# Kernel optimization log

Measured on AMD Instinct MI355X. Metric: run time of the kernel, lower is better.

The kernel has to match this reference:

```python
import jax, jax.numpy as jnp
import numpy as np
import math

B, S = 2, 2048
V, D, H, L, DFF = 1024, 512, 8, 6, 2048
DK = D // H
EPS = 1e-5


def _pos_encoding(seq_len, d_model, dtype):
    pos = jnp.arange(seq_len, dtype=jnp.float32)[:, None]
    div = jnp.exp(jnp.arange(0, d_model, 2, dtype=jnp.float32) * (-math.log(10000.0) / d_model))
    pe = jnp.zeros((seq_len, d_model), dtype=jnp.float32)
    pe = pe.at[:, 0::2].set(jnp.sin(pos * div))
    pe = pe.at[:, 1::2].set(jnp.cos(pos * div))
    return pe.astype(dtype)


def _layernorm(x, w, b):
    mu = jnp.mean(x, axis=-1, keepdims=True)
    var = jnp.mean(jnp.square(x - mu), axis=-1, keepdims=True)
    return (x - mu) * jax.lax.rsqrt(var + EPS) * w + b


def setup_inputs() -> dict:
    key = jax.random.key(0)
    ks = jax.random.split(key, 20)
    s = 0.02
    inp = {
        "input_ids": jax.random.randint(ks[0], (B, S), 1, V),
        "emb": jax.random.normal(ks[1], (V, D)) * s,
        # linear weights stored (in, out) so y = x @ W + b
        "wq": jax.random.normal(ks[2], (L, D, D)) * s,
        "bq": jnp.zeros((L, D)),
        "wk": jax.random.normal(ks[3], (L, D, D)) * s,
        "bk": jnp.zeros((L, D)),
        "wv": jax.random.normal(ks[4], (L, D, D)) * s,
        "bv": jnp.zeros((L, D)),
        "wo": jax.random.normal(ks[5], (L, D, D)) * (s / math.sqrt(2 * L)),
        "bo": jnp.zeros((L, D)),
        "ln1_w": jnp.ones((L, D)), "ln1_b": jnp.zeros((L, D)),
        "ln2_w": jnp.ones((L, D)), "ln2_b": jnp.zeros((L, D)),
        "w1": jax.random.normal(ks[6], (L, D, DFF)) * s,
        "b1": jnp.zeros((L, DFF)),
        "w2": jax.random.normal(ks[7], (L, DFF, D)) * (s / math.sqrt(2 * L)),
        "b2": jnp.zeros((L, D)),
        "out_w": jax.random.normal(ks[8], (D, V)) * s,
        "out_b": jnp.zeros((V,)),
    }
    return inp


def reference(input_ids, emb, wq, bq, wk, bk, wv, bv, wo, bo,
              ln1_w, ln1_b, ln2_w, ln2_b, w1, b1, w2, b2, out_w, out_b):
    pad_mask = (input_ids != 0)                              # [B,S] attend where True
    x = emb[input_ids]                                       # [B,S,D]
    x = x + _pos_encoding(S, D, x.dtype)[None, :, :]
    causal = jnp.tril(jnp.ones((S, S), dtype=bool))          # [S,S]
    mask = causal[None, None, :, :] & pad_mask[:, None, None, :]  # [B,1,S,S]
    scale = 1.0 / math.sqrt(DK)
    for l in range(L):
        h = _layernorm(x, ln1_w[l], ln1_b[l])
        q = (h @ wq[l] + bq[l]).reshape(B, S, H, DK)
        k = (h @ wk[l] + bk[l]).reshape(B, S, H, DK)
        v = (h @ wv[l] + bv[l]).reshape(B, S, H, DK)
        scores = jnp.einsum('bqhd,bkhd->bhqk', q, k) * scale
        scores = jnp.where(mask, scores, -jnp.inf)
        attn = jax.nn.softmax(scores, axis=-1)
        o = jnp.einsum('bhqk,bkhd->bqhd', attn, v).reshape(B, S, D)
        x = o @ wo[l] + bo[l]                                # NOTE: no residual on attention (faithful)
        h2 = _layernorm(x, ln2_w[l], ln2_b[l])
        ff = jax.nn.relu(h2 @ w1[l] + b1[l]) @ w2[l] + b2[l]
        x = x + ff
    logits = x @ out_w + out_b                               # [B,S,V]
    return logits
```

## Files before the change

### kernel.cpp

```cpp
#include <hip/hip_runtime.h>
#include <hip/hip_bf16.h>

#define B_ 2
#define S_ 2048
#define V_ 1024
#define D_ 512
#define H_ 8
#define L_ 6
#define DFF_ 2048
#define DK_ 64
#define MROWS (B_*S_)
#define NEGINF (-__builtin_inff())

typedef __hip_bfloat16 bf16;
typedef __bf16 bf16x8 __attribute__((ext_vector_type(8)));
typedef float f32x4 __attribute__((ext_vector_type(4)));
typedef unsigned short us8 __attribute__((ext_vector_type(8)));
typedef unsigned short us2 __attribute__((ext_vector_type(2)));

__device__ __forceinline__ float bf2f(unsigned short u) {
    return __uint_as_float(((unsigned int)u) << 16);
}
__device__ __forceinline__ unsigned short f2b(float x) {
    unsigned int u = __float_as_uint(x);
    return (unsigned short)((u + 0x7FFFu + ((u >> 16) & 1u)) >> 16);
}
__device__ __forceinline__ float ldin(const void* p, size_t i, int bf) {
    return bf ? bf2f(((const unsigned short*)p)[i]) : ((const float*)p)[i];
}

__global__ void detect_kernel(const unsigned int* __restrict__ w, int* __restrict__ flag) {
    if (threadIdx.x == 0) flag[0] = (w[0] == 0x3F800000u) ? 0 : 1;
}

__global__ __launch_bounds__(256) void embed_kernel(const int* __restrict__ ids,
        const void* __restrict__ emb, float* __restrict__ x, const int* __restrict__ dtf)
{
    const int bf = dtf[0];
    int tid = blockIdx.x * 256 + threadIdx.x;
    int d = tid % D_;
    int bs = tid / D_;
    int s = bs % S_;
    int id = ids[bs];
    float e = ldin(emb, (size_t)id * D_ + d, bf);
    int i2 = d & ~1;
    float div = expf((float)i2 * (-9.210340371976184f / (float)D_));
    float ang = (float)s * div;
    float pe = (d & 1) ? cosf(ang) : sinf(ang);
    x[tid] = e + pe;
}

__global__ __launch_bounds__(256) void ln_kernel(const float* __restrict__ x,
        const void* __restrict__ w, const void* __restrict__ b, size_t off,
        unsigned short* __restrict__ out, const int* __restrict__ dtf)
{
    const int bf = dtf[0];
    __shared__ float red[256];
    const int row = blockIdx.x;
    const int tid = threadIdx.x;
    const float* xr = x + (size_t)row * D_;
    float v0 = xr[tid], v1 = xr[tid + 256];
    red[tid] = v0 + v1; __syncthreads();
    for (int s = 128; s > 0; s >>= 1) { if (tid < s) red[tid] += red[tid + s]; __syncthreads(); }
    float mu = red[0] * (1.f / D_); __syncthreads();
    float d0 = v0 - mu, d1 = v1 - mu;
    red[tid] = d0 * d0 + d1 * d1; __syncthreads();
    for (int s = 128; s > 0; s >>= 1) { if (tid < s) red[tid] += red[tid + s]; __syncthreads(); }
    float var = red[0] * (1.f / D_);
    float rstd = rsqrtf(var + 1e-5f);
    unsigned short* orow = out + (size_t)row * D_;
    orow[tid]       = f2b(d0 * rstd * ldin(w, off + tid, bf)       + ldin(b, off + tid, bf));
    orow[tid + 256] = f2b(d1 * rstd * ldin(w, off + tid + 256, bf) + ldin(b, off + tid + 256, bf));
}

__device__ __forceinline__ void tr_tile(const void* src, size_t off, int K, int N,
        unsigned short* dst, int k0, int n0, int bf, unsigned short (*T)[72])
{
    const int t = threadIdx.x;
    const int r = t >> 2, c = (t & 3) * 16;
    size_t e = off + (size_t)(k0 + r) * N + n0 + c;
    us8 u0, u1;
    if (bf) {
        u0 = *(const us8*)((const unsigned short*)src + e);
        u1 = *(const us8*)((const unsigned short*)src + e + 8);
    } else {
        const float* p = (const float*)src + e;
        float4 f0 = *(const float4*)p, f1 = *(const float4*)(p + 4);
        float4 f2 = *(const float4*)(p + 8), f3 = *(const float4*)(p + 12);
        u0[0]=f2b(f0.x); u0[1]=f2b(f0.y); u0[2]=f2b(f0.z); u0[3]=f2b(f0.w);
        u0[4]=f2b(f1.x); u0[5]=f2b(f1.y); u0[6]=f2b(f1.z); u0[7]=f2b(f1.w);
        u1[0]=f2b(f2.x); u1[1]=f2b(f2.y); u1[2]=f2b(f2.z); u1[3]=f2b(f2.w);
        u1[4]=f2b(f3.x); u1[5]=f2b(f3.y); u1[6]=f2b(f3.z); u1[7]=f2b(f3.w);
    }
    *(us8*)&T[r][c] = u0;
    *(us8*)&T[r][c + 8] = u1;
    __syncthreads();
    us8 o0, o1;
    #pragma unroll
    for (int i = 0; i < 8; ++i) { o0[i] = T[c + i][r]; o1[i] = T[c + 8 + i][r]; }
    *(us8*)&dst[(size_t)(n0 + r) * K + k0 + c] = o0;
    *(us8*)&dst[(size_t)(n0 + r) * K + k0 + c + 8] = o1;
}

__global__ __launch_bounds__(256) void transpose_all(
        const void* wq, const void* wk, const void* wv, const void* wo,
        const void* w1, const void* w2,
        unsigned short* twq, unsigned short* twk, unsigned short* twv, unsigned short* two,
        unsigned short* tw1, unsigned short* tw2,
        int lbase, int slotmul, const int* __restrict__ dtf)
{
    __shared__ __align__(16) unsigned short T[64][72];
    const int bf = dtf[0];
    const int lrel = blockIdx.x / 768;
    const int within = blockIdx.x % 768;
    const int layer = lbase + lrel;
    const int slot = lrel * slotmul;
    const size_t offQ = (size_t)layer * D_ * D_;
    const size_t offF = (size_t)layer * D_ * DFF_;
    const size_t sQ = (size_t)slot * D_ * D_;
    const size_t sF = (size_t)slot * D_ * DFF_;
    if (within < 256) {
        int sel = within >> 6, tile = within & 63;
        const void* s = sel == 0 ? wq : sel == 1 ? wk : sel == 2 ? wv : wo;
        unsigned short* d = (sel == 0 ? twq : sel == 1 ? twk : sel == 2 ? twv : two) + sQ;
        tr_tile(s, offQ, D_, D_, d, (tile & 7) * 64, (tile >> 3) * 64, bf, T);
    } else if (within < 512) {
        int tile = within - 256;
        tr_tile(w1, offF, D_, DFF_, tw1 + sF, (tile & 7) * 64, (tile >> 3) * 64, bf, T);
    } else {
        int tile = within - 512;
        tr_tile(w2, offF, DFF_, D_, tw2 + sF, (tile & 31) * 64, (tile >> 5) * 64, bf, T);
    }
}

__global__ __launch_bounds__(256) void transpose_one(const void* src, size_t off,
        int K, int N, unsigned short* dst, const int* __restrict__ dtf)
{
    __shared__ __align__(16) unsigned short T[64][72];
    int tile = blockIdx.x;
    int tk = K / 64;
    tr_tile(src, off, K, N, dst, (tile % tk) * 64, (tile / tk) * 64, dtf[0], T);
}

template<bool ABF16, int OUTM, bool RELU, bool ADD>
__device__ __forceinline__ void gemm_core64(
        const void* __restrict__ A, const unsigned short* __restrict__ Wt,
        const void* __restrict__ bias, size_t bOff, const float* __restrict__ Res,
        void* __restrict__ Cout, int M, int N, int K, int bf)
{
    __shared__ __align__(16) unsigned short At[64][72];
    __shared__ __align__(16) unsigned short Bt[64][72];
    const int tid = threadIdx.x;
    const int wave = tid >> 6, lane = tid & 63;
    const int quad = lane >> 4, l16 = lane & 15;
    const int wm = (wave >> 1) * 32, wn = (wave & 1) * 32;
    const int n0 = blockIdx.x * 64, m0 = blockIdx.y * 64;
    const int r = tid >> 2, cb = tid & 3;

    f32x4 acc[2][2];
    #pragma unroll
    for (int mt = 0; mt < 2; ++mt)
        #pragma unroll
        for (int nt = 0; nt < 2; ++nt)
            acc[mt][nt] = (f32x4){0.f, 0.f, 0.f, 0.f};

    us8 aR[2], wR[2];
    float4 aF[4];

    auto loadT = [&](int k0) {
        if (ABF16) {
            const unsigned short* Ap = (const unsigned short*)A + (size_t)(m0 + r) * K + k0;
            aR[0] = *(const us8*)(Ap + cb * 8);
            aR[1] = *(const us8*)(Ap + (cb + 4) * 8);
        } else {
            const float* Ap = (const float*)A + (size_t)(m0 + r) * K + k0;
            aF[0] = *(const float4*)(Ap + cb * 8);
            aF[1] = *(const float4*)(Ap + cb * 8 + 4);
            aF[2] = *(const float4*)(Ap + (cb + 4) * 8);
            aF[3] = *(const float4*)(Ap + (cb + 4) * 8 + 4);
        }
        const unsigned short* Wp = Wt + (size_t)(n0 + r) * K + k0;
        wR[0] = *(const us8*)(Wp + cb * 8);
        wR[1] = *(const us8*)(Wp + (cb + 4) * 8);
    };
    auto storeT = [&]() {
        if (ABF16) {
            *(us8*)&At[r][cb * 8] = aR[0];
            *(us8*)&At[r][(cb + 4) * 8] = aR[1];
        } else {
            us8 u0, u1;
            u0[0]=f2b(aF[0].x); u0[1]=f2b(aF[0].y); u0[2]=f2b(aF[0].z); u0[3]=f2b(aF[0].w);
            u0[4]=f2b(aF[1].x); u0[5]=f2b(aF[1].y); u0[6]=f2b(aF[1].z); u0[7]=f2b(aF[1].w);
            u1[0]=f2b(aF[2].x); u1[1]=f2b(aF[2].y); u1[2]=f2b(aF[2].z); u1[3]=f2b(aF[2].w);
            u1[4]=f2b(aF[3].x); u1[5]=f2b(aF[3].y); u1[6]=f2b(aF[3].z); u1[7]=f2b(aF[3].w);
            *(us8*)&At[r][cb * 8] = u0;
            *(us8*)&At[r][(cb + 4) * 8] = u1;
        }
        *(us8*)&Bt[r][cb * 8] = wR[0];
        *(us8*)&Bt[r][(cb + 4) * 8] = wR[1];
    };

    loadT(0);
    for (int k0 = 0; k0 < K; k0 += 64) {
        __syncthreads();
        storeT();
        __syncthreads();
        if (k0 + 64 < K) loadT(k0 + 64);
        bf16x8 af[2][2], bw[2][2];
        #pragma unroll
        for (int mt = 0; mt < 2; ++mt)
            #pragma unroll
            for (int kh = 0; kh < 2; ++kh)
                af[mt][kh] = *(const bf16x8*)&At[wm + mt * 16 + l16][kh * 32 + quad * 8];
        #pragma unroll
        for (int nt = 0; nt < 2; ++nt)
            #pragma unroll
            for (int kh = 0; kh < 2; ++kh)
                bw[nt][kh] = *(const bf16x8*)&Bt[wn + nt * 16 + l16][kh * 32 + quad * 8];
        #pragma unroll
        for (int mt = 0; mt < 2; ++mt)
            #pragma unroll
            for (int nt = 0; nt < 2; ++nt) {
                acc[mt][nt] = __builtin_amdgcn_mfma_f32_16x16x32_bf16(af[mt][0], bw[nt][0], acc[mt][nt], 0, 0, 0);
                acc[mt][nt] = __builtin_amdgcn_mfma_f32_16x16x32_bf16(af[mt][1], bw[nt][1], acc[mt][nt], 0, 0, 0);
            }
    }

    #pragma unroll
    for (int mt = 0; mt < 2; ++mt) {
        #pragma unroll
        for (int nt = 0; nt < 2; ++nt) {
            int col = n0 + wn + nt * 16 + l16;
            float bv = ldin(bias, bOff + col, bf);
            #pragma unroll
            for (int rr = 0; rr < 4; ++rr) {
                int row = m0 + wm + mt * 16 + quad * 4 + rr;
                float c = acc[mt][nt][rr] + bv;
                if (ADD) c += Res[(size_t)row * N + col];
                if (RELU) c = fmaxf(c, 0.f);
                if (OUTM == 0)      ((float*)Cout)[(size_t)row * N + col] = c;
                else if (OUTM == 1) ((unsigned short*)Cout)[(size_t)row * N + col] = f2b(c);
                else {
                    if (bf) ((unsigned short*)Cout)[(size_t)row * N + col] = f2b(c);
                    else    ((float*)Cout)[(size_t)row * N + col] = c;
                }
            }
        }
    }
}

template<bool ABF16, int OUTM, bool RELU, bool ADD>
__global__ __launch_bounds__(256) void gemm64(
        const void* __restrict__ A, const unsigned short* __restrict__ Wt,
        const void* __restrict__ bias, size_t bOff, const float* __restrict__ Res,
        void* __restrict__ Cout, int M, int N, int K, const int* __restrict__ dtf)
{
    gemm_core64<ABF16, OUTM, RELU, ADD>(A, Wt, bias, bOff, Res, Cout, M, N, K, dtf[0]);
}

__global__ __launch_bounds__(256) void gemm_qkv64(
        const unsigned short* __restrict__ h,
        const unsigned short* twq, const unsigned short* twk, const unsigned short* twv,
        const void* bq, const void* bk, const void* bv, size_t bOff,
        unsigned short* q, unsigned short* k, unsigned short* v,
        const int* __restrict__ dtf)
{
    const int z = blockIdx.z;
    const unsigned short* W = (z == 0) ? twq : (z == 1) ? twk : twv;
    const void* bias = (z == 0) ? bq : (z == 1) ? bk : bv;
    unsigned short* out = (z == 0) ? q : (z == 1) ? k : v;
    gemm_core64<true, 1, false, false>(h, W, bias, bOff, nullptr, out, MROWS, D_, D_, dtf[0]);
}

__global__ __launch_bounds__(256) void attn_flash_v4(
        const unsigned short* __restrict__ qb, const unsigned short* __restrict__ kb,
        const unsigned short* __restrict__ vb, const int* __restrict__ ids,
        unsigned short* __restrict__ ob)
{
    __shared__ __align__(16) unsigned short Qs[64][72];
    __shared__ __align__(16) unsigned short Ks[2][64][72];
    __shared__ __align__(16) unsigned short Vt[2][64][72];
    __shared__ __align__(16) unsigned short Ps[64][72];
    __shared__ float Msk[S_];
    const int tid = threadIdx.x;
    const int wave = tid >> 6, lane = tid & 63;
    const int quad = lane >> 4, l16 = lane & 15;
    const int qt = 31 - blockIdx.x, h = blockIdx.y, b = blockIdx.z;
    const size_t hb = (size_t)b * S_ * D_ + (size_t)h * DK_;
    const int sr = tid >> 2, scq = (tid & 3) * 16;
    const int pr = tid >> 3, cvb = tid & 7;

    const int kcols = (qt + 1) * 64;
    for (int i = tid; i < kcols; i += 256)
        Msk[i] = (ids[b * S_ + i] == 0) ? NEGINF : 0.f;

    us8 kR0, kR1, vA, vB;
    auto loadKV = [&](int kt) {
        const unsigned short* kp = kb + hb + (size_t)(kt * 64 + sr) * D_ + scq;
        kR0 = *(const us8*)kp;
        kR1 = *(const us8*)(kp + 8);
        const unsigned short* vp = vb + hb + (size_t)(kt * 64 + 2 * pr) * D_ + cvb * 8;
        vA = *(const us8*)vp;
        vB = *(const us8*)(vp + D_);
    };
    auto storeKV = [&](int buf) {
        *(us8*)&Ks[buf][sr][scq]     = kR0;
        *(us8*)&Ks[buf][sr][scq + 8] = kR1;
        #pragma unroll
        for (int i = 0; i < 8; ++i) {
            int ii = (i + cvb) & 7;
            us2 u2 = { vA[ii], vB[ii] };
            *(us2*)&Vt[buf][cvb * 8 + ii][2 * pr] = u2;
        }
    };

    {
        const unsigned short* qp = qb + hb + (size_t)(qt * 64 + sr) * D_ + scq;
        *(us8*)&Qs[sr][scq]     = *(const us8*)qp;
        *(us8*)&Qs[sr][scq + 8] = *(const us8*)(qp + 8);
    }
    f32x4 Oa[4];
    float m[4], l[4];
    #pragma unroll
    for (int r = 0; r < 4; ++r) { m[r] = NEGINF; l[r] = 0.f; }
    #pragma unroll
    for (int dt = 0; dt < 4; ++dt) Oa[dt] = (f32x4){0.f, 0.f, 0.f, 0.f};

    loadKV(0);
    storeKV(0);
    if (qt >= 1) loadKV(1);
    __syncthreads();

    #pragma unroll 1
    for (int kt = 0; kt <= qt; ++kt) {
        const int cur = kt & 1;
        f32x4 sa[4];
        #pragma unroll
        for (int nt = 0; nt < 4; ++nt) sa[nt] = (f32x4){0.f, 0.f, 0.f, 0.f};
        #pragma unroll
        for (int ks = 0; ks < 2; ++ks) {
            bf16x8 aq = *(const bf16x8*)&Qs[wave * 16 + l16][ks * 32 + quad * 8];
            #pragma unroll
            for (int nt = 0; nt < 4; ++nt) {
                bf16x8 bk = *(const bf16x8*)&Ks[cur][nt * 16 + l16][ks * 32 + quad * 8];
                sa[nt] = __builtin_amdgcn_mfma_f32_16x16x32_bf16(aq, bk, sa[nt], 0, 0, 0);
            }
        }
        #pragma unroll
        for (int r = 0; r < 4; ++r) {
            float sv[4];
            #pragma unroll
            for (int nt = 0; nt < 4; ++nt) {
                float s = sa[nt][r] * 0.125f + Msk[kt * 64 + nt * 16 + l16];
                if (kt == qt && (nt * 16 + l16) > (wave * 16 + quad * 4 + r)) s = NEGINF;
                sv[nt] = s;
            }
            float rmax = fmaxf(fmaxf(sv[0], sv[1]), fmaxf(sv[2], sv[3]));
            #pragma unroll
            for (int off = 8; off > 0; off >>= 1)
                rmax = fmaxf(rmax, __shfl_xor(rmax, off, 16));
            float mnew = fmaxf(m[r], rmax);
            float alpha = __expf(m[r] - mnew);
            float p[4];
            float rsum = 0.f;
            #pragma unroll
            for (int nt = 0; nt < 4; ++nt) { p[nt] = __expf(sv[nt] - mnew); rsum += p[nt]; }
            #pragma unroll
            for (int off = 8; off > 0; off >>= 1)
                rsum += __shfl_xor(rsum, off, 16);
            l[r] = l[r] * alpha + rsum;
            m[r] = mnew;
            #pragma unroll
            for (int dt = 0; dt < 4; ++dt) Oa[dt][r] *= alpha;
            int prow = wave * 16 + quad * 4 + r;
            #pragma unroll
            for (int nt = 0; nt < 4; ++nt)
                Ps[prow][nt * 16 + l16] = f2b(p[nt]);
        }
        #pragma unroll
        for (int ks = 0; ks < 2; ++ks) {
            bf16x8 ap = *(const bf16x8*)&Ps[wave * 16 + l16][ks * 32 + quad * 8];
            #pragma unroll
            for (int dt = 0; dt < 4; ++dt) {
                bf16x8 bv = *(const bf16x8*)&Vt[cur][dt * 16 + l16][ks * 32 + quad * 8];
                Oa[dt] = __builtin_amdgcn_mfma_f32_16x16x32_bf16(ap, bv, Oa[dt], 0, 0, 0);
            }
        }
        if (kt + 1 <= qt) {
            storeKV(cur ^ 1);
            if (kt + 2 <= qt) loadKV(kt + 2);
            __syncthreads();
        }
    }
    #pragma unroll
    for (int r = 0; r < 4; ++r) {
        float inv = 1.f / l[r];
        int row = qt * 64 + wave * 16 + quad * 4 + r;
        #pragma unroll
        for (int dt = 0; dt < 4; ++dt)
            ob[hb + (size_t)row * D_ + dt * 16 + l16] = f2b(Oa[dt][r] * inv);
    }
}

extern "C" void kernel_launch(void* const* d_in, const int* in_sizes, int n_in,
                              void* d_out, int out_size, void* d_ws, size_t ws_size,
                              hipStream_t stream)
{
    const int* ids  = (const int*)d_in[0];
    const void* emb = d_in[1];
    const void* wq  = d_in[2];
    const void* bq  = d_in[3];
    const void* wk  = d_in[4];
    const void* bk  = d_in[5];
    const void* wv  = d_in[6];
    const void* bv  = d_in[7];
    const void* wo  = d_in[8];
    const void* bo  = d_in[9];
    const void* ln1w = d_in[10];
    const void* ln1b = d_in[11];
    const void* ln2w = d_in[12];
    const void* ln2b = d_in[13];
    const void* w1  = d_in[14];
    const void* b1  = d_in[15];
    const void* w2  = d_in[16];
    const void* b2  = d_in[17];
    const void* outw = d_in[18];
    const void* outb = d_in[19];

    char* wsp = (char*)d_ws;
    int* dtf = (int*)wsp;
    const size_t NROW = (size_t)MROWS * D_;

    const size_t fixedBytes = 256
        + 2 * NROW * 4
        + 5 * NROW * 2
        + (size_t)MROWS * DFF_ * 2
        + (size_t)D_ * V_ * 2;
    const size_t perLayerW = (4 * (size_t)D_ * D_ + 2 * (size_t)D_ * DFF_) * 2;
    const int slots = (ws_size >= fixedBytes + 6 * perLayerW) ? 6 : 1;

    float* xA = (float*)(wsp + 256);
    float* xB = xA + NROW;
    unsigned short* h  = (unsigned short*)(xB + NROW);
    unsigned short* q  = h + NROW;
    unsigned short* k  = q + NROW;
    unsigned short* v  = k + NROW;
    unsigned short* o  = v + NROW;
    unsigned short* ff = o + NROW;
    unsigned short* twout = ff + (size_t)MROWS * DFF_;
    unsigned short* twq = twout + (size_t)D_ * V_;
    unsigned short* twk = twq + (size_t)slots * D_ * D_;
    unsigned short* twv = twk + (size_t)slots * D_ * D_;
    unsigned short* two = twv + (size_t)slots * D_ * D_;
    unsigned short* tw1 = two + (size_t)slots * D_ * D_;
    unsigned short* tw2 = tw1 + (size_t)slots * D_ * DFF_;

    detect_kernel<<<1, 64, 0, stream>>>((const unsigned int*)ln1w, dtf);
    transpose_one<<<(D_/64) * (V_/64), 256, 0, stream>>>(outw, 0, D_, V_, twout, dtf);
    if (slots == 6)
        transpose_all<<<6 * 768, 256, 0, stream>>>(wq, wk, wv, wo, w1, w2,
            twq, twk, twv, two, tw1, tw2, 0, 1, dtf);
    embed_kernel<<<(MROWS * D_) / 256, 256, 0, stream>>>(ids, emb, xA, dtf);

    for (int l = 0; l < L_; ++l) {
        const size_t bOff = (size_t)l * D_;
        const int s = (slots == 6) ? l : 0;
        if (slots == 1)
            transpose_all<<<768, 256, 0, stream>>>(wq, wk, wv, wo, w1, w2,
                twq, twk, twv, two, tw1, tw2, l, 0, dtf);
        const unsigned short* lwq = twq + (size_t)s * D_ * D_;
        const unsigned short* lwk = twk + (size_t)s * D_ * D_;
        const unsigned short* lwv = twv + (size_t)s * D_ * D_;
        const unsigned short* lwo = two + (size_t)s * D_ * D_;
        const unsigned short* lw1 = tw1 + (size_t)s * D_ * DFF_;
        const unsigned short* lw2 = tw2 + (size_t)s * D_ * DFF_;

        ln_kernel<<<MROWS, 256, 0, stream>>>(xA, ln1w, ln1b, bOff, h, dtf);
        gemm_qkv64<<<dim3(D_/64, MROWS/64, 3), 256, 0, stream>>>(
            h, lwq, lwk, lwv, bq, bk, bv, bOff, q, k, v, dtf);
        attn_flash_v4<<<dim3(S_/64, H_, B_), 256, 0, stream>>>(q, k, v, ids, o);
        gemm64<true, 0, false, false><<<dim3(D_/64, MROWS/64), 256, 0, stream>>>(
            o, lwo, bo, bOff, nullptr, xB, MROWS, D_, D_, dtf);
        ln_kernel<<<MROWS, 256, 0, stream>>>(xB, ln2w, ln2b, bOff, h, dtf);
        gemm64<true, 1, true, false><<<dim3(DFF_/64, MROWS/64), 256, 0, stream>>>(
            h, lw1, b1, (size_t)l * DFF_, nullptr, ff, MROWS, DFF_, D_, dtf);
        gemm64<true, 0, false, true><<<dim3(D_/64, MROWS/64), 256, 0, stream>>>(
            ff, lw2, b2, bOff, xB, xA, MROWS, D_, DFF_, dtf);
    }
    gemm64<false, 2, false, false><<<dim3(V_/64, MROWS/64), 256, 0, stream>>>(
        xA, twout, outb, 0, nullptr, d_out, MROWS, V_, D_, dtf);
}
```

Baseline: 1.160 ms.

## Pre-transpose V and stream K/V from global directly in flash attention

Adds a separate kernel that transposes V per batch and head into a head-major layout (reusing the ff buffer). The attention kernel drops its shared-memory Q/K/V staging and block barriers: Q stays in registers, and K and transposed V fragments are loaded straight from global memory into MFMA operands. It computes S transposed so each lane owns one query row, which simplifies the row max and sum reductions, and adds s_setprio around the MFMA sections. The aim is to remove LDS traffic and __syncthreads stalls, at the cost of an extra launch and relying on L2/cache for K/V reuse across the four waves.

```diff
diff --git a/kernel.cpp b/kernel.cpp
--- a/kernel.cpp
+++ b/kernel.cpp
@@ -16,7 +16,7 @@
 typedef __bf16 bf16x8 __attribute__((ext_vector_type(8)));
 typedef float f32x4 __attribute__((ext_vector_type(4)));
 typedef unsigned short us8 __attribute__((ext_vector_type(8)));
-typedef unsigned short us2 __attribute__((ext_vector_type(2)));
+typedef unsigned short us4 __attribute__((ext_vector_type(4)));
 
 __device__ __forceinline__ float bf2f(unsigned short u) {
     return __uint_as_float(((unsigned int)u) << 16);
@@ -142,6 +142,15 @@
     tr_tile(src, off, K, N, dst, (tile % tk) * 64, (tile / tk) * 64, dtf[0], T);
 }
 
+__global__ __launch_bounds__(256) void transpose_vt(
+        const unsigned short* __restrict__ v, unsigned short* __restrict__ vt)
+{
+    __shared__ __align__(16) unsigned short T[64][72];
+    tr_tile(v, (size_t)blockIdx.z * S_ * D_ + blockIdx.y * DK_, S_, D_,
+            vt + (size_t)(blockIdx.z * H_ + blockIdx.y) * DK_ * S_,
+            blockIdx.x * 64, 0, 1, T);
+}
+
 template<bool ABF16, int OUTM, bool RELU, bool ADD>
 __device__ __forceinline__ void gemm_core64(
         const void* __restrict__ A, const unsigned short* __restrict__ Wt,
@@ -272,129 +281,109 @@
     gemm_core64<true, 1, false, false>(h, W, bias, bOff, nullptr, out, MROWS, D_, D_, dtf[0]);
 }
 
-__global__ __launch_bounds__(256) void attn_flash_v4(
+__global__ __launch_bounds__(256) void attn_flash_v7(
         const unsigned short* __restrict__ qb, const unsigned short* __restrict__ kb,
-        const unsigned short* __restrict__ vb, const int* __restrict__ ids,
+        const unsigned short* __restrict__ vt, const int* __restrict__ ids,
         unsigned short* __restrict__ ob)
 {
-    __shared__ __align__(16) unsigned short Qs[64][72];
-    __shared__ __align__(16) unsigned short Ks[2][64][72];
-    __shared__ __align__(16) unsigned short Vt[2][64][72];
-    __shared__ __align__(16) unsigned short Ps[64][72];
+    __shared__ __align__(16) unsigned short Ps[4][16][72];
     __shared__ float Msk[S_];
     const int tid = threadIdx.x;
     const int wave = tid >> 6, lane = tid & 63;
     const int quad = lane >> 4, l16 = lane & 15;
-    const int qt = 31 - blockIdx.x, h = blockIdx.y, b = blockIdx.z;
-    const size_t hb = (size_t)b * S_ * D_ + (size_t)h * DK_;
-    const int sr = tid >> 2, scq = (tid & 3) * 16;
-    const int pr = tid >> 3, cvb = tid & 7;
+    const int qt = 31 - blockIdx.x, h = blockIdx.y, bz = blockIdx.z;
+    const size_t hb = (size_t)bz * S_ * D_ + (size_t)h * DK_;
+    const unsigned short* vbh = vt + (size_t)(bz * H_ + h) * DK_ * S_;
+    const int qrow = qt * 64 + wave * 16 + l16;
 
     const int kcols = (qt + 1) * 64;
     for (int i = tid; i < kcols; i += 256)
-        Msk[i] = (ids[b * S_ + i] == 0) ? NEGINF : 0.f;
-
-    us8 kR0, kR1, vA, vB;
-    auto loadKV = [&](int kt) {
-        const unsigned short* kp = kb + hb + (size_t)(kt * 64 + sr) * D_ + scq;
-        kR0 = *(const us8*)kp;
-        kR1 = *(const us8*)(kp + 8);
-        const unsigned short* vp = vb + hb + (size_t)(kt * 64 + 2 * pr) * D_ + cvb * 8;
-        vA = *(const us8*)vp;
-        vB = *(const us8*)(vp + D_);
-    };
-    auto storeKV = [&](int buf) {
-        *(us8*)&Ks[buf][sr][scq]     = kR0;
-        *(us8*)&Ks[buf][sr][scq + 8] = kR1;
-        #pragma unroll
-        for (int i = 0; i < 8; ++i) {
-            int ii = (i + cvb) & 7;
-            us2 u2 = { vA[ii], vB[ii] };
-            *(us2*)&Vt[buf][cvb * 8 + ii][2 * pr] = u2;
-        }
-    };
-
-    {
-        const unsigned short* qp = qb + hb + (size_t)(qt * 64 + sr) * D_ + scq;
-        *(us8*)&Qs[sr][scq]     = *(const us8*)qp;
-        *(us8*)&Qs[sr][scq + 8] = *(const us8*)(qp + 8);
-    }
+        Msk[i] = (ids[bz * S_ + i] == 0) ? NEGINF : 0.f;
+    __syncthreads();
+
+    bf16x8 aq[2];
+    #pragma unroll
+    for (int ks = 0; ks < 2; ++ks)
+        aq[ks] = *(const bf16x8*)(qb + hb + (size_t)qrow * D_ + ks * 32 + quad * 8);
+
     f32x4 Oa[4];
-    float m[4], l[4];
-    #pragma unroll
-    for (int r = 0; r < 4; ++r) { m[r] = NEGINF; l[r] = 0.f; }
+    float m_s = NEGINF, l_s = 0.f;
     #pragma unroll
     for (int dt = 0; dt < 4; ++dt) Oa[dt] = (f32x4){0.f, 0.f, 0.f, 0.f};
-
-    loadKV(0);
-    storeKV(0);
-    if (qt >= 1) loadKV(1);
-    __syncthreads();
 
     #pragma unroll 1
     for (int kt = 0; kt <= qt; ++kt) {
-        const int cur = kt & 1;
-        f32x4 sa[4];
-        #pragma unroll
-        for (int nt = 0; nt < 4; ++nt) sa[nt] = (f32x4){0.f, 0.f, 0.f, 0.f};
+        const bool causal = (kt == qt);
+        f32x4 sw[4];
+        #pragma unroll
+        for (int nt = 0; nt < 4; ++nt) sw[nt] = (f32x4){0.f, 0.f, 0.f, 0.f};
+        __builtin_amdgcn_s_setprio(1);
         #pragma unroll
         for (int ks = 0; ks < 2; ++ks) {
-            bf16x8 aq = *(const bf16x8*)&Qs[wave * 16 + l16][ks * 32 + quad * 8];
             #pragma unroll
             for (int nt = 0; nt < 4; ++nt) {
-                bf16x8 bk = *(const bf16x8*)&Ks[cur][nt * 16 + l16][ks * 32 + quad * 8];
-                sa[nt] = __builtin_amdgcn_mfma_f32_16x16x32_bf16(aq, bk, sa[nt], 0, 0, 0);
-            }
-        }
+                bf16x8 bk = *(const bf16x8*)(kb + hb +
+                        (size_t)(kt * 64 + nt * 16 + l16) * D_ + ks * 32 + quad * 8);
+                sw[nt] = __builtin_amdgcn_mfma_f32_16x16x32_bf16(bk, aq[ks], sw[nt], 0, 0, 0);
+            }
+        }
+        __builtin_amdgcn_s_setprio(0);
+        float sv[4][4];
+        float tmax = NEGINF;
+        #pragma unroll
+        for (int nt = 0; nt < 4; ++nt) {
+            f32x4 mskv = *(const f32x4*)&Msk[kt * 64 + nt * 16 + quad * 4];
+            #pragma unroll
+            for (int rr = 0; rr < 4; ++rr) {
+                float s = sw[nt][rr] * 0.125f + mskv[rr];
+                if (causal && (nt * 16 + quad * 4 + rr) > (wave * 16 + l16)) s = NEGINF;
+                sv[nt][rr] = s;
+                tmax = fmaxf(tmax, s);
+            }
+        }
+        tmax = fmaxf(tmax, __shfl_xor(tmax, 16));
+        tmax = fmaxf(tmax, __shfl_xor(tmax, 32));
+        float mnew = fmaxf(m_s, tmax);
+        float alpha = __expf(m_s - mnew);
+        float rsum = 0.f;
+        #pragma unroll
+        for (int nt = 0; nt < 4; ++nt) {
+            us4 pk;
+            #pragma unroll
+            for (int rr = 0; rr < 4; ++rr) {
+                float pv = __expf(sv[nt][rr] - mnew);
+                rsum += pv;
+                pk[rr] = f2b(pv);
+            }
+            *(us4*)&Ps[wave][l16][nt * 16 + quad * 4] = pk;
+        }
+        rsum += __shfl_xor(rsum, 16);
+        rsum += __shfl_xor(rsum, 32);
+        l_s = l_s * alpha + rsum;
+        m_s = mnew;
         #pragma unroll
         for (int r = 0; r < 4; ++r) {
-            float sv[4];
-            #pragma unroll
-            for (int nt = 0; nt < 4; ++nt) {
-                float s = sa[nt][r] * 0.125f + Msk[kt * 64 + nt * 16 + l16];
-                if (kt == qt && (nt * 16 + l16) > (wave * 16 + quad * 4 + r)) s = NEGINF;
-                sv[nt] = s;
-            }
-            float rmax = fmaxf(fmaxf(sv[0], sv[1]), fmaxf(sv[2], sv[3]));
-            #pragma unroll
-            for (int off = 8; off > 0; off >>= 1)
-                rmax = fmaxf(rmax, __shfl_xor(rmax, off, 16));
-            float mnew = fmaxf(m[r], rmax);
-            float alpha = __expf(m[r] - mnew);
-            float p[4];
-            float rsum = 0.f;
-            #pragma unroll
-            for (int nt = 0; nt < 4; ++nt) { p[nt] = __expf(sv[nt] - mnew); rsum += p[nt]; }
-            #pragma unroll
-            for (int off = 8; off > 0; off >>= 1)
-                rsum += __shfl_xor(rsum, off, 16);
-            l[r] = l[r] * alpha + rsum;
-            m[r] = mnew;
-            #pragma unroll
-            for (int dt = 0; dt < 4; ++dt) Oa[dt][r] *= alpha;
-            int prow = wave * 16 + quad * 4 + r;
-            #pragma unroll
-            for (int nt = 0; nt < 4; ++nt)
-                Ps[prow][nt * 16 + l16] = f2b(p[nt]);
-        }
+            float ar = __shfl(alpha, quad * 4 + r, 16);
+            #pragma unroll
+            for (int dt = 0; dt < 4; ++dt) Oa[dt][r] *= ar;
+        }
+        __builtin_amdgcn_s_setprio(1);
         #pragma unroll
         for (int ks = 0; ks < 2; ++ks) {
-            bf16x8 ap = *(const bf16x8*)&Ps[wave * 16 + l16][ks * 32 + quad * 8];
+            bf16x8 ap = *(const bf16x8*)&Ps[wave][l16][ks * 32 + quad * 8];
             #pragma unroll
             for (int dt = 0; dt < 4; ++dt) {
-                bf16x8 bv = *(const bf16x8*)&Vt[cur][dt * 16 + l16][ks * 32 + quad * 8];
+                bf16x8 bv = *(const bf16x8*)(vbh +
+                        (size_t)(dt * 16 + l16) * S_ + kt * 64 + ks * 32 + quad * 8);
                 Oa[dt] = __builtin_amdgcn_mfma_f32_16x16x32_bf16(ap, bv, Oa[dt], 0, 0, 0);
             }
         }
-        if (kt + 1 <= qt) {
-            storeKV(cur ^ 1);
-            if (kt + 2 <= qt) loadKV(kt + 2);
-            __syncthreads();
-        }
+        __builtin_amdgcn_s_setprio(0);
     }
     #pragma unroll
     for (int r = 0; r < 4; ++r) {
-        float inv = 1.f / l[r];
+        float lr = __shfl(l_s, quad * 4 + r, 16);
+        float inv = 1.f / lr;
         int row = qt * 64 + wave * 16 + quad * 4 + r;
         #pragma unroll
         for (int dt = 0; dt < 4; ++dt)
@@ -454,6 +443,7 @@
     unsigned short* two = twv + (size_t)slots * D_ * D_;
     unsigned short* tw1 = two + (size_t)slots * D_ * D_;
     unsigned short* tw2 = tw1 + (size_t)slots * D_ * DFF_;
+    unsigned short* vt = ff;
 
     detect_kernel<<<1, 64, 0, stream>>>((const unsigned int*)ln1w, dtf);
     transpose_one<<<(D_/64) * (V_/64), 256, 0, stream>>>(outw, 0, D_, V_, twout, dtf);
@@ -478,7 +468,8 @@
         ln_kernel<<<MROWS, 256, 0, stream>>>(xA, ln1w, ln1b, bOff, h, dtf);
         gemm_qkv64<<<dim3(D_/64, MROWS/64, 3), 256, 0, stream>>>(
             h, lwq, lwk, lwv, bq, bk, bv, bOff, q, k, v, dtf);
-        attn_flash_v4<<<dim3(S_/64, H_, B_), 256, 0, stream>>>(q, k, v, ids, o);
+        transpose_vt<<<dim3(S_/64, H_, B_), 256, 0, stream>>>(v, vt);
+        attn_flash_v7<<<dim3(S_/64, H_, B_), 256, 0, stream>>>(q, k, vt, ids, o);
         gemm64<true, 0, false, false><<<dim3(D_/64, MROWS/64), 256, 0, stream>>>(
             o, lwo, bo, bOff, nullptr, xB, MROWS, D_, D_, dtf);
         ln_kernel<<<MROWS, 256, 0, stream>>>(xB, ln2w, ln2b, bOff, h, dtf);
```

After: 1.576 ms. 1.36x slower.
